# Optimization experiments

Hardware: AMD Instinct MI355X
Metric: run time of the kernel (lower is better)

The kernel has to match this reference:

```python
import jax, jax.numpy as jnp
import numpy as np

# global prototype index ranges per scale: scale s owns protos [s0, s1)
SCALES = ((0, 100), (100, 200))
NEG = jnp.float32(-1e30)


def _scale_terms(d, lab_flat, cls_of):
    """d: [B,P,Hs,Ws] distances for this scale; lab_flat: [B,N] downsampled labels
    (already shifted by -1); cls_of: [P] class id of each local prototype.
    Returns (sum of exp(-sym_kld) over valid prototype pairs, number of valid pairs).
    """
    B, P = d.shape[0], d.shape[1]
    dflat = d.reshape(B, P, -1)                                   # [B,P,N]
    M = lab_flat[:, None, :] == cls_of[None, :, None]             # [B,P,N] pixel mask per proto's class
    count = M.sum(-1)                                             # [B,P] masked pixel count
    # masked log_softmax over the class pixels of each prototype
    lse = jax.nn.logsumexp(jnp.where(M, dflat, NEG), axis=-1)     # [B,P]
    L = jnp.where(M, dflat - lse[:, :, None], 0.0)                # log-probs on mask, 0 elsewhere
    Pr = jnp.where(M, jnp.exp(L), 0.0)                            # probs on mask, 0 elsewhere
    E = jnp.sum(Pr * L, axis=-1)                                  # [B,P] sum p*log p
    # Cmat[b,a,c] = sum_n Pr[b,a,n] * L[b,c,n]
    Cmat = jnp.einsum('ban,bcn->bac', Pr, L)                      # [B,P,P]
    # sym_kld[b,j,k] = 0.5*((E_k - sum p_k log p_j) + (E_j - sum p_j log p_k))
    kld = 0.5 * (E[:, None, :] + E[:, :, None] - Cmat - jnp.swapaxes(Cmat, 1, 2))
    idx = jnp.arange(P)
    same = (cls_of[:, None] == cls_of[None, :]) & (idx[:, None] < idx[None, :])  # j<k, same class
    valid = same[None] & (count[:, :, None] >= 2) & (count[:, None, :] >= 2)      # need >=2 masked pixels
    return jnp.sum(jnp.where(valid, jnp.exp(-kld), 0.0)), jnp.sum(valid)


def reference(dist0, dist1, target_labels, proto_class):
    lab = target_labels - 1                                       # [B,H,W], -1 = ignore
    B, H, W = lab.shape
    tot = jnp.float32(0.0)
    cnt = jnp.int32(0)
    for d, (s0, s1) in zip((dist0, dist1), SCALES):
        Hs, Ws = d.shape[2], d.shape[3]
        # torch F.interpolate(mode='nearest'): src index = floor(dst * in/out)
        ri = (jnp.arange(Hs) * H) // Hs
        ci = (jnp.arange(Ws) * W) // Ws
        lab_flat = lab[:, ri][:, :, ci].reshape(B, Hs * Ws)
        s, n = _scale_terms(d, lab_flat, proto_class[s0:s1])
        tot = tot + s
        cnt = cnt + n
    return jnp.where(cnt > 0, tot / jnp.maximum(cnt, 1).astype(jnp.float32), jnp.float32(0.0))


def setup_inputs() -> dict:
    key = jax.random.key(0)
    k0, k1, k2 = jax.random.split(key, 3)
    B, C, PPC = 16, 20, 5  # batch, num classes, protos per class per scale
    dist0 = jax.random.normal(k0, (B, 100, 128, 128), dtype=jnp.float32)
    dist1 = jax.random.normal(k1, (B, 100, 64, 64), dtype=jnp.float32)
    # labels in 1..C ; 0 becomes -1 after the shift and is ignored
    target_labels = jax.random.randint(k2, (B, 512, 512), 0, C + 1).astype(jnp.int32)
    proto_class = ((jnp.arange(200) % 100) // PPC).astype(jnp.int32)
    return {"dist0": dist0, "dist1": dist1, "target_labels": target_labels, "proto_class": proto_class}
```

## Files before the change

kernel.cpp:

```cpp
#include <hip/hip_runtime.h>
#include <math.h>

#define TPB 256
#define NCLS 20
#define PPC 5
#define NB 16
#define N0 16384
#define N1 4096
#define RECSZ 32
#define NWA 3200
#define NBLKB 640

__global__ void downsample_labels(const int* __restrict__ tgt,
                                  char* __restrict__ lab0, char* __restrict__ lab1) {
    const int q = blockIdx.x * blockDim.x + threadIdx.x;
    if (q < 65536) {
        const int b = q >> 12, r = q & 4095;
        const int i = r >> 5, j0 = (r & 31) << 2;
        const int* src = tgt + b * 262144 + (i << 2) * 512;
        char4 v;
        v.x = (char)(src[(j0 + 0) << 2] - 1);
        v.y = (char)(src[(j0 + 1) << 2] - 1);
        v.z = (char)(src[(j0 + 2) << 2] - 1);
        v.w = (char)(src[(j0 + 3) << 2] - 1);
        ((char4*)lab0)[q] = v;
    } else {
        const int k = q - 65536;
        const int b = k >> 10, r = k & 1023;
        const int i = r >> 4, j0 = (r & 15) << 2;
        const int* src = tgt + b * 262144 + (i << 3) * 512;
        char4 v;
        v.x = (char)(src[(j0 + 0) << 3] - 1);
        v.y = (char)(src[(j0 + 1) << 3] - 1);
        v.z = (char)(src[(j0 + 2) << 3] - 1);
        v.w = (char)(src[(j0 + 3) << 3] - 1);
        ((char4*)lab1)[k] = v;
    }
}

__global__ __launch_bounds__(64) void kA(const float* __restrict__ dist0,
                                         const float* __restrict__ dist1,
                                         const char* __restrict__ lab0,
                                         const char* __restrict__ lab1,
                                         float* __restrict__ recs) {
    const int blk = blockIdx.x;
    int scale, bc, seg;
    if (blk < 2560) { scale = 0; bc = blk >> 3; seg = blk & 7; }
    else            { const int k = blk - 2560; scale = 1; bc = k >> 1; seg = k & 1; }
    const int b = bc / NCLS, c = bc % NCLS;
    const int N = scale ? N1 : N0;
    const float* dist = scale ? dist1 : dist0;
    const char* lab = (scale ? lab1 + b * N1 : lab0 + b * N0) + seg * 2048;
    const float* base = dist + (size_t)(b * 100 + c * PPC) * N + seg * 2048;

    const int lane = threadIdx.x;
    const float4* r0 = (const float4*)(base);
    const float4* r1 = (const float4*)(base + N);
    const float4* r2 = (const float4*)(base + 2 * N);
    const float4* r3 = (const float4*)(base + 3 * N);
    const float4* r4 = (const float4*)(base + 4 * N);
    const char4* lab4 = (const char4*)lab;

    float s[PPC] = {0.f, 0.f, 0.f, 0.f, 0.f};
    float T1[25];
#pragma unroll
    for (int i = 0; i < 25; ++i) T1[i] = 0.f;
    int kcnt = 0;

    char4 L = lab4[lane];
    float4 A0 = r0[lane], A1 = r1[lane], A2 = r2[lane], A3 = r3[lane], A4 = r4[lane];

#pragma unroll
    for (int it = 0; it < 8; ++it) {
        char4 Ln;
        float4 B0, B1, B2, B3, B4;
        if (it < 7) {
            const int ni = (it + 1) * 64 + lane;
            Ln = lab4[ni];
            B0 = r0[ni]; B1 = r1[ni]; B2 = r2[ni]; B3 = r3[ni]; B4 = r4[ni];
        }
#define DO_E(F)                                                                  \
        if ((int)L.F == c) {                                                     \
            float dv[PPC] = {A0.F, A1.F, A2.F, A3.F, A4.F};                      \
            float ev[PPC];                                                       \
            _Pragma("unroll")                                                    \
            for (int p = 0; p < PPC; ++p) { ev[p] = __expf(dv[p]); s[p] += ev[p]; } \
            _Pragma("unroll")                                                    \
            for (int aa = 0; aa < PPC; ++aa)                                     \
            _Pragma("unroll")                                                    \
                for (int bb = 0; bb < PPC; ++bb)                                 \
                    T1[aa * PPC + bb] = fmaf(ev[aa], dv[bb], T1[aa * PPC + bb]); \
            ++kcnt;                                                              \
        }
        DO_E(x) DO_E(y) DO_E(z) DO_E(w)
#undef DO_E
        L = Ln; A0 = B0; A1 = B1; A2 = B2; A3 = B3; A4 = B4;
    }

    float kc = (float)kcnt;
#pragma unroll
    for (int d = 32; d >= 1; d >>= 1) {
#pragma unroll
        for (int p = 0; p < PPC; ++p) s[p] += __shfl_xor(s[p], d, 64);
#pragma unroll
        for (int i = 0; i < 25; ++i) T1[i] += __shfl_xor(T1[i], d, 64);
        kc += __shfl_xor(kc, d, 64);
    }

    if (lane == 0) {
        float* r = recs + (size_t)blk * RECSZ;
#pragma unroll
        for (int p = 0; p < PPC; ++p) r[p] = s[p];
#pragma unroll
        for (int i = 0; i < 25; ++i) r[5 + i] = T1[i];
        r[30] = kc;
    }
}

__global__ __launch_bounds__(64) void kB(const float* __restrict__ recs,
                                         float* __restrict__ psum,
                                         float* __restrict__ pcnt) {
    const int blk = blockIdx.x;
    const int lane = threadIdx.x;
    const int scale = (blk >= 320) ? 1 : 0;
    const int bc = blk - scale * 320;
    const int rbase = scale ? (2560 + bc * 2) : (bc * 8);
    const int nrec = scale ? 2 : 8;
    const int a = (lane < 25) ? lane / 5 : 0;
    const int bb = (lane < 25) ? lane % 5 : 0;

    float S = 0.f, U = 0.f, cnt = 0.f;
    if (lane < 5)
        for (int r = 0; r < nrec; ++r) S += recs[(size_t)(rbase + r) * RECSZ + lane];
    if (lane < 25)
        for (int r = 0; r < nrec; ++r) U += recs[(size_t)(rbase + r) * RECSZ + 5 + lane];
    if (lane == 0)
        for (int r = 0; r < nrec; ++r) cnt += recs[(size_t)(rbase + r) * RECSZ + 30];
    cnt = __shfl(cnt, 0, 64);

    const float lse = (lane < 5) ? logf(S) : 0.f;
    const float Sa    = __shfl(S, a, 64);
    const float lse_b = __shfl(lse, bb, 64);
    const float C = U / Sa - lse_b;

    float tot = 0.f;
#pragma unroll
    for (int j = 0; j < PPC; ++j)
#pragma unroll
        for (int k = j + 1; k < PPC; ++k) {
            const float Ejj = __shfl(C, j * 5 + j, 64);
            const float Ekk = __shfl(C, k * 5 + k, 64);
            const float Cjk = __shfl(C, j * 5 + k, 64);
            const float Ckj = __shfl(C, k * 5 + j, 64);
            tot += expf(-0.5f * (Ejj + Ekk - Cjk - Ckj));
        }
    if (lane == 0) {
        const bool ok = (cnt >= 2.f);
        psum[blk] = ok ? tot : 0.f;
        pcnt[blk] = ok ? 10.f : 0.f;
    }
}

__global__ void finalize_kernel(const float* __restrict__ psum,
                                const float* __restrict__ pcnt,
                                float* __restrict__ out) {
    __shared__ float rs[TPB], rc[TPB];
    const int tid = threadIdx.x;
    float s = 0.f, c = 0.f;
    for (int i = tid; i < NBLKB; i += TPB) { s += psum[i]; c += pcnt[i]; }
    rs[tid] = s; rc[tid] = c;
    __syncthreads();
    for (int off = 128; off > 0; off >>= 1) {
        if (tid < off) { rs[tid] += rs[tid + off]; rc[tid] += rc[tid + off]; }
        __syncthreads();
    }
    if (tid == 0) out[0] = (rc[0] > 0.f) ? (rs[0] / rc[0]) : 0.f;
}

extern "C" void kernel_launch(void* const* d_in, const int* in_sizes, int n_in,
                              void* d_out, int out_size, void* d_ws, size_t ws_size,
                              hipStream_t stream) {
    const float* dist0 = (const float*)d_in[0];
    const float* dist1 = (const float*)d_in[1];
    const int*   tgt   = (const int*)d_in[2];
    float* out = (float*)d_out;

    char*  lab0 = (char*)d_ws;
    char*  lab1 = lab0 + 262144;
    float* recs = (float*)(lab0 + 327680);
    float* psum = recs + (size_t)NWA * RECSZ;
    float* pcnt = psum + NBLKB;

    downsample_labels<<<320, TPB, 0, stream>>>(tgt, lab0, lab1);
    kA<<<NWA, 64, 0, stream>>>(dist0, dist1, lab0, lab1, recs);
    kB<<<NBLKB, 64, 0, stream>>>(recs, psum, pcnt);
    finalize_kernel<<<1, TPB, 0, stream>>>(psum, pcnt, out);
}
```

Measured before the change: 43.86 us.

## Split kA into twice as many smaller segments with branchless masked accumulation

Doubles the number of kA blocks so each wave handles 1024 pixels per prototype group instead of 2048, and updates kB's record indexing to match. The per-pixel class test becomes a multiply by a 0/1 weight instead of a divergent branch, and launch bounds now request 4 waves per SIMD to limit register use. The aim is more waves in flight to hide memory latency and no divergence. In exchange it computes exp and FMAs for every pixel, not just masked ones, and doubles the cross-lane reductions and record writes.

```diff
diff --git a/kernel.cpp b/kernel.cpp
--- a/kernel.cpp
+++ b/kernel.cpp
@@ -8,7 +8,7 @@
 #define N0 16384
 #define N1 4096
 #define RECSZ 32
-#define NWA 3200
+#define NWA 6400
 #define NBLKB 640
 
 __global__ void downsample_labels(const int* __restrict__ tgt,
@@ -38,20 +38,20 @@
     }
 }
 
-__global__ __launch_bounds__(64) void kA(const float* __restrict__ dist0,
-                                         const float* __restrict__ dist1,
-                                         const char* __restrict__ lab0,
-                                         const char* __restrict__ lab1,
-                                         float* __restrict__ recs) {
+__global__ __launch_bounds__(64, 4) void kA(const float* __restrict__ dist0,
+                                            const float* __restrict__ dist1,
+                                            const char* __restrict__ lab0,
+                                            const char* __restrict__ lab1,
+                                            float* __restrict__ recs) {
     const int blk = blockIdx.x;
     int scale, bc, seg;
-    if (blk < 2560) { scale = 0; bc = blk >> 3; seg = blk & 7; }
-    else            { const int k = blk - 2560; scale = 1; bc = k >> 1; seg = k & 1; }
+    if (blk < 5120) { scale = 0; bc = blk >> 4; seg = blk & 15; }
+    else            { const int k = blk - 5120; scale = 1; bc = k >> 2; seg = k & 3; }
     const int b = bc / NCLS, c = bc % NCLS;
     const int N = scale ? N1 : N0;
     const float* dist = scale ? dist1 : dist0;
-    const char* lab = (scale ? lab1 + b * N1 : lab0 + b * N0) + seg * 2048;
-    const float* base = dist + (size_t)(b * 100 + c * PPC) * N + seg * 2048;
+    const char* lab = (scale ? lab1 + b * N1 : lab0 + b * N0) + seg * 1024;
+    const float* base = dist + (size_t)(b * 100 + c * PPC) * N + seg * 1024;
 
     const int lane = threadIdx.x;
     const float4* r0 = (const float4*)(base);
@@ -61,56 +61,68 @@
     const float4* r4 = (const float4*)(base + 4 * N);
     const char4* lab4 = (const char4*)lab;
 
-    float s[PPC] = {0.f, 0.f, 0.f, 0.f, 0.f};
+    float s0 = 0.f, s1 = 0.f, s2 = 0.f, s3 = 0.f, s4 = 0.f, kc = 0.f;
     float T1[25];
 #pragma unroll
     for (int i = 0; i < 25; ++i) T1[i] = 0.f;
-    int kcnt = 0;
-
-    char4 L = lab4[lane];
-    float4 A0 = r0[lane], A1 = r1[lane], A2 = r2[lane], A3 = r3[lane], A4 = r4[lane];
-
-#pragma unroll
-    for (int it = 0; it < 8; ++it) {
-        char4 Ln;
-        float4 B0, B1, B2, B3, B4;
-        if (it < 7) {
-            const int ni = (it + 1) * 64 + lane;
-            Ln = lab4[ni];
-            B0 = r0[ni]; B1 = r1[ni]; B2 = r2[ni]; B3 = r3[ni]; B4 = r4[ni];
-        }
-#define DO_E(F)                                                                  \
-        if ((int)L.F == c) {                                                     \
-            float dv[PPC] = {A0.F, A1.F, A2.F, A3.F, A4.F};                      \
-            float ev[PPC];                                                       \
-            _Pragma("unroll")                                                    \
-            for (int p = 0; p < PPC; ++p) { ev[p] = __expf(dv[p]); s[p] += ev[p]; } \
-            _Pragma("unroll")                                                    \
-            for (int aa = 0; aa < PPC; ++aa)                                     \
-            _Pragma("unroll")                                                    \
-                for (int bb = 0; bb < PPC; ++bb)                                 \
-                    T1[aa * PPC + bb] = fmaf(ev[aa], dv[bb], T1[aa * PPC + bb]); \
-            ++kcnt;                                                              \
-        }
-        DO_E(x) DO_E(y) DO_E(z) DO_E(w)
-#undef DO_E
-        L = Ln; A0 = B0; A1 = B1; A2 = B2; A3 = B3; A4 = B4;
-    }
-
-    float kc = (float)kcnt;
+
+    char4  cL = lab4[lane];
+    float4 c0 = r0[lane], c1 = r1[lane], c2 = r2[lane], c3 = r3[lane], c4 = r4[lane];
+
+#define SLOT(F)                                                                  \
+    {                                                                            \
+        const float w  = ((int)cL.F == c) ? 1.f : 0.f;                           \
+        const float d0 = c0.F, d1 = c1.F, d2 = c2.F, d3 = c3.F, d4 = c4.F;       \
+        const float e0 = __expf(d0) * w, e1 = __expf(d1) * w,                    \
+                    e2 = __expf(d2) * w, e3 = __expf(d3) * w,                    \
+                    e4 = __expf(d4) * w;                                         \
+        s0 += e0; s1 += e1; s2 += e2; s3 += e3; s4 += e4; kc += w;               \
+        T1[0]  = fmaf(e0, d0, T1[0]);  T1[1]  = fmaf(e0, d1, T1[1]);             \
+        T1[2]  = fmaf(e0, d2, T1[2]);  T1[3]  = fmaf(e0, d3, T1[3]);             \
+        T1[4]  = fmaf(e0, d4, T1[4]);                                            \
+        T1[5]  = fmaf(e1, d0, T1[5]);  T1[6]  = fmaf(e1, d1, T1[6]);             \
+        T1[7]  = fmaf(e1, d2, T1[7]);  T1[8]  = fmaf(e1, d3, T1[8]);             \
+        T1[9]  = fmaf(e1, d4, T1[9]);                                            \
+        T1[10] = fmaf(e2, d0, T1[10]); T1[11] = fmaf(e2, d1, T1[11]);            \
+        T1[12] = fmaf(e2, d2, T1[12]); T1[13] = fmaf(e2, d3, T1[13]);            \
+        T1[14] = fmaf(e2, d4, T1[14]);                                           \
+        T1[15] = fmaf(e3, d0, T1[15]); T1[16] = fmaf(e3, d1, T1[16]);            \
+        T1[17] = fmaf(e3, d2, T1[17]); T1[18] = fmaf(e3, d3, T1[18]);            \
+        T1[19] = fmaf(e3, d4, T1[19]);                                           \
+        T1[20] = fmaf(e4, d0, T1[20]); T1[21] = fmaf(e4, d1, T1[21]);            \
+        T1[22] = fmaf(e4, d2, T1[22]); T1[23] = fmaf(e4, d3, T1[23]);            \
+        T1[24] = fmaf(e4, d4, T1[24]);                                           \
+    }
+
+#define ITER_PF(NI)                                                              \
+    {                                                                            \
+        const int ni = (NI) * 64 + lane;                                         \
+        const char4  nL = lab4[ni];                                              \
+        const float4 n0 = r0[ni], n1 = r1[ni], n2 = r2[ni],                      \
+                     n3 = r3[ni], n4 = r4[ni];                                   \
+        SLOT(x) SLOT(y) SLOT(z) SLOT(w)                                          \
+        cL = nL; c0 = n0; c1 = n1; c2 = n2; c3 = n3; c4 = n4;                    \
+    }
+
+    ITER_PF(1)
+    ITER_PF(2)
+    ITER_PF(3)
+    SLOT(x) SLOT(y) SLOT(z) SLOT(w)
+#undef ITER_PF
+#undef SLOT
+
 #pragma unroll
     for (int d = 32; d >= 1; d >>= 1) {
-#pragma unroll
-        for (int p = 0; p < PPC; ++p) s[p] += __shfl_xor(s[p], d, 64);
+        s0 += __shfl_xor(s0, d, 64); s1 += __shfl_xor(s1, d, 64);
+        s2 += __shfl_xor(s2, d, 64); s3 += __shfl_xor(s3, d, 64);
+        s4 += __shfl_xor(s4, d, 64); kc += __shfl_xor(kc, d, 64);
 #pragma unroll
         for (int i = 0; i < 25; ++i) T1[i] += __shfl_xor(T1[i], d, 64);
-        kc += __shfl_xor(kc, d, 64);
     }
 
     if (lane == 0) {
         float* r = recs + (size_t)blk * RECSZ;
-#pragma unroll
-        for (int p = 0; p < PPC; ++p) r[p] = s[p];
+        r[0] = s0; r[1] = s1; r[2] = s2; r[3] = s3; r[4] = s4;
 #pragma unroll
         for (int i = 0; i < 25; ++i) r[5 + i] = T1[i];
         r[30] = kc;
@@ -124,8 +136,8 @@
     const int lane = threadIdx.x;
     const int scale = (blk >= 320) ? 1 : 0;
     const int bc = blk - scale * 320;
-    const int rbase = scale ? (2560 + bc * 2) : (bc * 8);
-    const int nrec = scale ? 2 : 8;
+    const int rbase = scale ? (5120 + bc * 4) : (bc * 16);
+    const int nrec = scale ? 4 : 16;
     const int a = (lane < 25) ? lane / 5 : 0;
     const int bb = (lane < 25) ? lane % 5 : 0;
 
```

New measurement: 115.2 us. 2.63x slower.
